# Kernel optimization log

Hardware: AMD Instinct MI355X
Metric: run time of the kernel (lower is better)

## Reference

```python
import jax, jax.numpy as jnp
import numpy as np

PROJ_SCALE = 0.1


def setup_inputs() -> dict:
    key = jax.random.key(0)
    ks = jax.random.split(key, 6)
    B, D, K, E = 8192, 256, 63, 64  # batch, n_features, num_breakpoints, emb_dim_per_feature
    x_num = jax.random.normal(ks[0], (B, D), dtype=jnp.float32)
    basis_weight = jax.random.normal(ks[1], (D, K + 1, E), dtype=jnp.float32) * 0.001
    basis_bias = jnp.zeros((D, E), dtype=jnp.float32)
    proj_w = jax.random.normal(ks[2], (D, D * E), dtype=jnp.float32) * 0.01  # torch Linear weight (out, in)
    proj_b = jnp.zeros((D,), dtype=jnp.float32)
    breakpoint_min = jax.random.normal(ks[3], (D, 1), dtype=jnp.float32) * 0.1
    breakpoint_delta_raw = jax.random.normal(ks[4], (D, K), dtype=jnp.float32) * 0.5
    return {
        "x_num": x_num,
        "basis_weight": basis_weight,
        "basis_bias": basis_bias,
        "proj_w": proj_w,
        "proj_b": proj_b,
        "breakpoint_min": breakpoint_min,
        "breakpoint_delta_raw": breakpoint_delta_raw,
    }


def reference(x_num, basis_weight, basis_bias, proj_w, proj_b, breakpoint_min, breakpoint_delta_raw):
    # breakpoints: monotone via softplus deltas + cumsum, shape [D, K]
    deltas = jax.nn.softplus(breakpoint_delta_raw)
    breakpoints = breakpoint_min + jnp.cumsum(deltas, axis=1)
    # piecewise-linear basis: [B, D, K+1]
    basis = jax.nn.relu(x_num[:, :, None] - breakpoints[None, :, :])
    basis = jnp.concatenate([x_num[:, :, None], basis], axis=-1)
    # per-feature batched matmul: [B, D, E]
    embeddings = jnp.einsum("bdf,dfe->bde", basis, basis_weight) + basis_bias
    flat = embeddings.reshape(x_num.shape[0], -1)  # [B, D*E]
    x_emb = x_num + PROJ_SCALE * (flat @ proj_w.T + proj_b)
    return x_emb, embeddings, breakpoints
```

## Files before the change

kernel.cpp:

```cpp
#include <hip/hip_runtime.h>
#include <hip/hip_bf16.h>

#define NB 8192
#define ND 256
#define NKBP 63
#define NF 64
#define NE 64
#define NKP 16384
#define NDE 16384
#define NSPLIT 8

typedef __attribute__((ext_vector_type(8))) short short8_t;
typedef __attribute__((ext_vector_type(4))) short short4_t;
typedef __attribute__((ext_vector_type(4))) float f32x4;

__device__ __forceinline__ unsigned short bfbits(float v) {
  union { __hip_bfloat16 b; unsigned short u; } cv;
  cv.b = __float2bfloat16(v);
  return cv.u;
}
__device__ __forceinline__ float bf2f(unsigned short s) {
  return __uint_as_float(((unsigned)s) << 16);
}

__global__ void k_maxx(const float* __restrict__ x, float* __restrict__ bmax) {
  const int t = threadIdx.x;
  const float* px = x + (size_t)blockIdx.x * 8192;
  float m = 0.f;
  #pragma unroll 4
  for (int i = t; i < 8192; i += 256) m = fmaxf(m, px[i]);
  #pragma unroll
  for (int off = 32; off > 0; off >>= 1) m = fmaxf(m, __shfl_down(m, off, 64));
  __shared__ float red[4];
  if ((t & 63) == 0) red[t >> 6] = m;
  __syncthreads();
  if (t == 0) bmax[blockIdx.x] = fmaxf(fmaxf(red[0], red[1]), fmaxf(red[2], red[3]));
}

__global__ void k_bp(const float* __restrict__ bmin, const float* __restrict__ draw,
                     const float* __restrict__ bmax, float* __restrict__ obp,
                     int* __restrict__ fdv, int* __restrict__ fcutc) {
  const int d = threadIdx.x;
  __shared__ float mred[256];
  __shared__ int fds[256];
  mred[d] = bmax[d];
  __syncthreads();
  for (int s = 128; s > 0; s >>= 1) {
    if (d < s) mred[d] = fmaxf(mred[d], mred[d + s]);
    __syncthreads();
  }
  const float maxx = mred[0];
  float a = bmin[d];
  int cnt = 0;
  for (int j = 0; j < NKBP; ++j) {
    float r = draw[d * NKBP + j];
    a += fmaxf(r, 0.f) + log1pf(expf(-fabsf(r)));
    obp[d * NKBP + j] = a;
    cnt += (a < maxx) ? 1 : 0;
  }
  const int Fd = 1 + cnt;
  fdv[d] = Fd;
  fds[d] = Fd;
  __syncthreads();
  if (d < NSPLIT) {
    int mx = 0;
    for (int k = 0; k < 32; ++k) mx = max(mx, fds[d * 32 + k]);
    fcutc[d] = (mx > 32) ? 2 : 1;
  }
}

__global__ __launch_bounds__(256, 2) void k_w2(
    const float* __restrict__ bw, const float* __restrict__ pw,
    const float* __restrict__ bb, unsigned short* __restrict__ w2f,
    float* __restrict__ cb_part) {
  const int d = blockIdx.x;
  const int t = threadIdx.x;
  const int l = t & 63, w = t >> 6;
  const int lr = l & 15, lg = l >> 4;
  __shared__ unsigned short pwS[256 * 72];
  __shared__ unsigned short bwS[64 * 72];
  __shared__ float bbS[64];

  {
    const int rr = t >> 4, e0 = (t & 15) * 4;
    #pragma unroll
    for (int it = 0; it < 16; ++it) {
      const int n = it * 16 + rr;
      f32x4 v = *(const f32x4*)(pw + (size_t)n * NDE + d * 64 + e0);
      short4_t s;
      s[0] = (short)bfbits(v[0]); s[1] = (short)bfbits(v[1]);
      s[2] = (short)bfbits(v[2]); s[3] = (short)bfbits(v[3]);
      *(short4_t*)(pwS + n * 72 + e0) = s;
    }
    #pragma unroll
    for (int it = 0; it < 4; ++it) {
      const int f = it * 16 + rr;
      f32x4 v = *(const f32x4*)(bw + (size_t)d * 4096 + f * 64 + e0);
      short4_t s;
      s[0] = (short)bfbits(v[0]); s[1] = (short)bfbits(v[1]);
      s[2] = (short)bfbits(v[2]); s[3] = (short)bfbits(v[3]);
      *(short4_t*)(bwS + f * 72 + e0) = s;
    }
    if (t < 64) bbS[t] = bb[(size_t)d * 64 + t];
  }
  __syncthreads();

  f32x4 acc[4][4];
  #pragma unroll
  for (int mi = 0; mi < 4; ++mi)
    #pragma unroll
    for (int ni = 0; ni < 4; ++ni) acc[mi][ni] = (f32x4){0.f, 0.f, 0.f, 0.f};

  short8_t afr[4][2], bfr[4][2];
  #pragma unroll
  for (int kf = 0; kf < 2; ++kf) {
    #pragma unroll
    for (int mi = 0; mi < 4; ++mi) {
      const int n = w * 64 + mi * 16 + lr;
      afr[mi][kf] = *(const short8_t*)(pwS + n * 72 + kf * 32 + lg * 8);
    }
    #pragma unroll
    for (int ni = 0; ni < 4; ++ni) {
      const int f = ni * 16 + lr;
      bfr[ni][kf] = *(const short8_t*)(bwS + f * 72 + kf * 32 + lg * 8);
    }
  }
  #pragma unroll
  for (int kf = 0; kf < 2; ++kf)
    #pragma unroll
    for (int mi = 0; mi < 4; ++mi)
      #pragma unroll
      for (int ni = 0; ni < 4; ++ni)
        acc[mi][ni] = __builtin_amdgcn_mfma_f32_16x16x32_bf16(afr[mi][kf], bfr[ni][kf], acc[mi][ni], 0, 0, 0);

  #pragma unroll
  for (int mi = 0; mi < 4; ++mi)
    #pragma unroll
    for (int ni = 0; ni < 4; ++ni) {
      const int kf_s = ni >> 1;
      const int lgp  = (ni * 2 + (lr >> 3)) & 3;
      const int jj   = lr & 7;
      const int nb   = w * 64 + mi * 16 + lg * 4;
      const size_t base = (((size_t)d * 2 + kf_s) * 4 + lgp) * 256;
      #pragma unroll
      for (int r = 0; r < 4; ++r)
        w2f[(base + (nb + r)) * 8 + jj] = bfbits(acc[mi][ni][r]);
    }

  {
    float cacc = 0.f;
    #pragma unroll 8
    for (int e = 0; e < 64; ++e) cacc += bf2f(pwS[t * 72 + e]) * bbS[e];
    cb_part[(size_t)d * 256 + t] = cacc;
  }
}

__global__ void k_cbr(const float* __restrict__ cb_part, float* __restrict__ c) {
  const int t = threadIdx.x;
  float a0 = 0.f, a1 = 0.f, a2 = 0.f, a3 = 0.f;
  for (int d = 0; d < ND; d += 4) {
    a0 += cb_part[(size_t)(d + 0) * 256 + t];
    a1 += cb_part[(size_t)(d + 1) * 256 + t];
    a2 += cb_part[(size_t)(d + 2) * 256 + t];
    a3 += cb_part[(size_t)(d + 3) * 256 + t];
  }
  c[t] = (a0 + a1) + (a2 + a3);
}

template<bool KF1>
__device__ __forceinline__ void proj_kloop(
    const unsigned short* const (&bbase)[4], const float* const (&xrow)[2],
    const float* thrS_lg, bool lg0, f32x4 (&acc)[2][4]) {
  for (int c = 0; c < 4; ++c) {
    f32x4 xqa[2], xqb[2];
    #pragma unroll
    for (int mi = 0; mi < 2; ++mi) {
      xqa[mi] = *(const f32x4*)(xrow[mi] + c * 8);
      xqb[mi] = *(const f32x4*)(xrow[mi] + c * 8 + 4);
    }
    #pragma unroll
    for (int dd = 0; dd < 8; ++dd) {
      const int dl = c * 8 + dd;
      short8_t bfr0[4], bfr1[4];
      #pragma unroll
      for (int ni = 0; ni < 4; ++ni)
        bfr0[ni] = *(const short8_t*)(bbase[ni] + (size_t)dl * 16384);
      if (KF1) {
        #pragma unroll
        for (int ni = 0; ni < 4; ++ni)
          bfr1[ni] = *(const short8_t*)(bbase[ni] + (size_t)dl * 16384 + 8192);
      }
      const float* tp = thrS_lg + dl * 64;
      f32x4 ta = *(const f32x4*)(tp);
      f32x4 tb = *(const f32x4*)(tp + 4);
      short8_t afr0[2], afr1[2];
      #pragma unroll
      for (int mi = 0; mi < 2; ++mi) {
        const float xv = (dd < 4) ? xqa[mi][dd & 3] : xqb[mi][dd & 3];
        short8_t A0;
        A0[0] = (short)bfbits(lg0 ? xv : fmaxf(xv - ta[0], 0.f));
        A0[1] = (short)bfbits(fmaxf(xv - ta[1], 0.f));
        A0[2] = (short)bfbits(fmaxf(xv - ta[2], 0.f));
        A0[3] = (short)bfbits(fmaxf(xv - ta[3], 0.f));
        A0[4] = (short)bfbits(fmaxf(xv - tb[0], 0.f));
        A0[5] = (short)bfbits(fmaxf(xv - tb[1], 0.f));
        A0[6] = (short)bfbits(fmaxf(xv - tb[2], 0.f));
        A0[7] = (short)bfbits(fmaxf(xv - tb[3], 0.f));
        afr0[mi] = A0;
      }
      if (KF1) {
        f32x4 tc = *(const f32x4*)(tp + 32);
        f32x4 td = *(const f32x4*)(tp + 36);
        #pragma unroll
        for (int mi = 0; mi < 2; ++mi) {
          const float xv = (dd < 4) ? xqa[mi][dd & 3] : xqb[mi][dd & 3];
          short8_t A1;
          A1[0] = (short)bfbits(fmaxf(xv - tc[0], 0.f));
          A1[1] = (short)bfbits(fmaxf(xv - tc[1], 0.f));
          A1[2] = (short)bfbits(fmaxf(xv - tc[2], 0.f));
          A1[3] = (short)bfbits(fmaxf(xv - tc[3], 0.f));
          A1[4] = (short)bfbits(fmaxf(xv - td[0], 0.f));
          A1[5] = (short)bfbits(fmaxf(xv - td[1], 0.f));
          A1[6] = (short)bfbits(fmaxf(xv - td[2], 0.f));
          A1[7] = (short)bfbits(fmaxf(xv - td[3], 0.f));
          afr1[mi] = A1;
        }
      }
      #pragma unroll
      for (int mi = 0; mi < 2; ++mi)
        #pragma unroll
        for (int ni = 0; ni < 4; ++ni)
          acc[mi][ni] = __builtin_amdgcn_mfma_f32_16x16x32_bf16(afr0[mi], bfr0[ni], acc[mi][ni], 0, 0, 0);
      if (KF1) {
        #pragma unroll
        for (int mi = 0; mi < 2; ++mi)
          #pragma unroll
          for (int ni = 0; ni < 4; ++ni)
            acc[mi][ni] = __builtin_amdgcn_mfma_f32_16x16x32_bf16(afr1[mi], bfr1[ni], acc[mi][ni], 0, 0, 0);
      }
    }
  }
}

__global__ __launch_bounds__(256, 3) void k_proj(
    const unsigned short* __restrict__ w2f, const float* __restrict__ bp,
    const float* __restrict__ x, const int* __restrict__ fcutc,
    float* __restrict__ pbuf) {
  const int t = threadIdx.x;
  const int l = t & 63, w = t >> 6;
  const int lr = l & 15, lg = l >> 4;
  const int bM = blockIdx.x * 128;
  const int bN = blockIdx.y * 64;
  const int d0 = blockIdx.z * 32;
  __shared__ float thrS[32 * 64];

  for (int i = t; i < 2048; i += 256) {
    const int dl = i >> 6, f = i & 63;
    thrS[i] = (f >= 1) ? bp[(size_t)(d0 + dl) * NKBP + f - 1] : 0.0f;
  }
  __syncthreads();

  f32x4 acc[2][4];
  #pragma unroll
  for (int mi = 0; mi < 2; ++mi)
    #pragma unroll
    for (int ni = 0; ni < 4; ++ni) acc[mi][ni] = (f32x4){0.f, 0.f, 0.f, 0.f};

  const bool lg0 = (lg == 0);
  const unsigned short* bbase[4];
  #pragma unroll
  for (int ni = 0; ni < 4; ++ni)
    bbase[ni] = w2f + (size_t)d0 * 16384 + (size_t)(bN + ni * 16 + lr) * 8 + (size_t)lg * 2048;
  const float* xrow[2];
  #pragma unroll
  for (int mi = 0; mi < 2; ++mi)
    xrow[mi] = x + (size_t)(bM + w * 32 + mi * 16 + lr) * ND + d0;

  const int nkf = fcutc[blockIdx.z];
  if (nkf == 1) proj_kloop<false>(bbase, xrow, thrS + lg * 8, lg0, acc);
  else          proj_kloop<true >(bbase, xrow, thrS + lg * 8, lg0, acc);

  float* pp = pbuf + (size_t)blockIdx.z * ((size_t)NB * ND);
  #pragma unroll
  for (int mi = 0; mi < 2; ++mi)
    #pragma unroll
    for (int ni = 0; ni < 4; ++ni) {
      const int col = bN + ni * 16 + lr;
      const int rowb = bM + w * 32 + mi * 16 + lg * 4;
      #pragma unroll
      for (int r = 0; r < 4; ++r)
        pp[(size_t)(rowb + r) * ND + col] = acc[mi][ni][r];
    }
}

__global__ void k_comb(const float* __restrict__ x, const float* __restrict__ pbuf,
                       const float* __restrict__ cbuf, const float* __restrict__ pb,
                       float* __restrict__ xe) {
  const size_t i = ((size_t)blockIdx.x * 256 + threadIdx.x) * 4;
  const int n = (int)(i & 255);
  f32x4 s = *(const f32x4*)(pbuf + i);
  #pragma unroll
  for (int p = 1; p < NSPLIT; ++p)
    s += *(const f32x4*)(pbuf + (size_t)p * 2097152 + i);
  f32x4 cv = *(const f32x4*)(cbuf + n);
  f32x4 pv = *(const f32x4*)(pb + n);
  f32x4 xv = *(const f32x4*)(x + i);
  *(f32x4*)(xe + i) = xv + 0.1f * (s + cv + pv);
}

__global__ __launch_bounds__(256, 2) void k_emb(
    const float* __restrict__ x, const float* __restrict__ bw,
    const float* __restrict__ bb, const float* __restrict__ bp,
    const int* __restrict__ fdv, float* __restrict__ oe) {
  const int d = blockIdx.y;
  const int b0 = blockIdx.x * 256;
  const int t = threadIdx.x;
  const int l = t & 63, w = t >> 6;
  const int lr = l & 15, lg = l >> 4;
  __shared__ unsigned short btS[64 * 72];
  __shared__ float thrF[64];
  __shared__ float bbS[64];
  __shared__ float cS[4 * 64 * 68];

  const int nkf = (fdv[d] > 32) ? 2 : 1;

  float xg[4];
  #pragma unroll
  for (int mi = 0; mi < 4; ++mi)
    xg[mi] = x[(size_t)(b0 + w * 64 + mi * 16 + lr) * ND + d];

  if (t < 64) thrF[t] = (t >= 1) ? bp[(size_t)d * NKBP + t - 1] : 0.0f;
  else if (t < 128) bbS[t - 64] = bb[(size_t)d * 64 + (t - 64)];
  {
    const float* bwd = bw + (size_t)d * 4096;
    const int f = t >> 2, e0 = (t & 3) * 16;
    #pragma unroll
    for (int q = 0; q < 4; ++q) {
      f32x4 v = *(const f32x4*)(bwd + f * 64 + e0 + q * 4);
      #pragma unroll
      for (int r = 0; r < 4; ++r) {
        const int e = e0 + q * 4 + r;
        btS[e * 72 + f] = bfbits(v[r]);
      }
    }
  }
  __syncthreads();

  f32x4 ta = *(const f32x4*)(thrF + lg * 8);
  f32x4 tb = *(const f32x4*)(thrF + lg * 8 + 4);
  const bool lg0 = (lg == 0);

  short8_t afr0[4], afr1[4];
  #pragma unroll
  for (int mi = 0; mi < 4; ++mi) {
    const float xv = xg[mi];
    short8_t A0;
    A0[0] = (short)bfbits(lg0 ? xv : fmaxf(xv - ta[0], 0.f));
    A0[1] = (short)bfbits(fmaxf(xv - ta[1], 0.f));
    A0[2] = (short)bfbits(fmaxf(xv - ta[2], 0.f));
    A0[3] = (short)bfbits(fmaxf(xv - ta[3], 0.f));
    A0[4] = (short)bfbits(fmaxf(xv - tb[0], 0.f));
    A0[5] = (short)bfbits(fmaxf(xv - tb[1], 0.f));
    A0[6] = (short)bfbits(fmaxf(xv - tb[2], 0.f));
    A0[7] = (short)bfbits(fmaxf(xv - tb[3], 0.f));
    afr0[mi] = A0;
  }
  short8_t bfr0[4], bfr1[4];
  #pragma unroll
  for (int ni = 0; ni < 4; ++ni) {
    const int e = ni * 16 + lr;
    bfr0[ni] = *(const short8_t*)(btS + e * 72 + lg * 8);
  }
  f32x4 acc[4][4];
  #pragma unroll
  for (int mi = 0; mi < 4; ++mi)
    #pragma unroll
    for (int ni = 0; ni < 4; ++ni) acc[mi][ni] = (f32x4){0.f, 0.f, 0.f, 0.f};
  #pragma unroll
  for (int mi = 0; mi < 4; ++mi)
    #pragma unroll
    for (int ni = 0; ni < 4; ++ni)
      acc[mi][ni] = __builtin_amdgcn_mfma_f32_16x16x32_bf16(afr0[mi], bfr0[ni], acc[mi][ni], 0, 0, 0);

  if (nkf == 2) {
    f32x4 tc = *(const f32x4*)(thrF + 32 + lg * 8);
    f32x4 td = *(const f32x4*)(thrF + 36 + lg * 8);
    #pragma unroll
    for (int mi = 0; mi < 4; ++mi) {
      const float xv = xg[mi];
      short8_t A1;
      A1[0] = (short)bfbits(fmaxf(xv - tc[0], 0.f));
      A1[1] = (short)bfbits(fmaxf(xv - tc[1], 0.f));
      A1[2] = (short)bfbits(fmaxf(xv - tc[2], 0.f));
      A1[3] = (short)bfbits(fmaxf(xv - tc[3], 0.f));
      A1[4] = (short)bfbits(fmaxf(xv - td[0], 0.f));
      A1[5] = (short)bfbits(fmaxf(xv - td[1], 0.f));
      A1[6] = (short)bfbits(fmaxf(xv - td[2], 0.f));
      A1[7] = (short)bfbits(fmaxf(xv - td[3], 0.f));
      afr1[mi] = A1;
    }
    #pragma unroll
    for (int ni = 0; ni < 4; ++ni) {
      const int e = ni * 16 + lr;
      bfr1[ni] = *(const short8_t*)(btS + e * 72 + 32 + lg * 8);
    }
    #pragma unroll
    for (int mi = 0; mi < 4; ++mi)
      #pragma unroll
      for (int ni = 0; ni < 4; ++ni)
        acc[mi][ni] = __builtin_amdgcn_mfma_f32_16x16x32_bf16(afr1[mi], bfr1[ni], acc[mi][ni], 0, 0, 0);
  }

  #pragma unroll
  for (int ni = 0; ni < 4; ++ni) {
    const float bbv = bbS[ni * 16 + lr];
    #pragma unroll
    for (int mi = 0; mi < 4; ++mi) {
      const int rw = mi * 16 + lg * 4;
      #pragma unroll
      for (int r = 0; r < 4; ++r)
        cS[w * 4352 + (rw + r) * 68 + ni * 16 + lr] = acc[mi][ni][r] + bbv;
    }
  }
  __syncthreads();

  const int rsub = t >> 4;
  const int c4 = (t & 15) * 4;
  #pragma unroll
  for (int p = 0; p < 16; ++p) {
    const int row = p * 16 + rsub;
    const int wsrc = row >> 6, wr = row & 63;
    f32x4 v = *(const f32x4*)(cS + wsrc * 4352 + wr * 68 + c4);
    *(f32x4*)(oe + (size_t)(b0 + row) * NDE + d * 64 + c4) = v;
  }
}

extern "C" void kernel_launch(void* const* d_in, const int* in_sizes, int n_in,
                              void* d_out, int out_size, void* d_ws, size_t ws_size,
                              hipStream_t stream) {
  const float* x    = (const float*)d_in[0];
  const float* bw   = (const float*)d_in[1];
  const float* bb   = (const float*)d_in[2];
  const float* pw   = (const float*)d_in[3];
  const float* pb   = (const float*)d_in[4];
  const float* bmin = (const float*)d_in[5];
  const float* draw = (const float*)d_in[6];

  float* out    = (float*)d_out;
  float* out_x  = out;
  float* out_e  = out + (size_t)NB * ND;
  float* out_bp = out_e + (size_t)NB * NDE;

  unsigned short* w2f = (unsigned short*)out_x;
  float* cbuf    = out_e;
  float* pbuf    = out_e + 65536;
  float* cb_part = out_e + 65536 + NSPLIT * 2097152;
  float* bmax = (float*)d_ws;
  int*   fdv  = (int*)d_ws + 256;
  int*   fcutc= (int*)d_ws + 512;

  k_maxx<<<dim3(256),          dim3(256), 0, stream>>>(x, bmax);
  k_bp  <<<dim3(1),            dim3(256), 0, stream>>>(bmin, draw, bmax, out_bp, fdv, fcutc);
  k_w2  <<<dim3(256),          dim3(256), 0, stream>>>(bw, pw, bb, w2f, cb_part);
  k_cbr <<<dim3(1),            dim3(256), 0, stream>>>(cb_part, cbuf);
  k_proj<<<dim3(64, 4, NSPLIT),dim3(256), 0, stream>>>(w2f, out_bp, x, fcutc, pbuf);
  k_comb<<<dim3(2048),         dim3(256), 0, stream>>>(x, pbuf, cbuf, pb, out_x);
  k_emb <<<dim3(32, 256),      dim3(256), 0, stream>>>(x, bw, bb, out_bp, fdv, out_e);
}
```

Before: 264.7 us.

## Skip unused K chunks in k_w2, prefetch proj B fragments, shrink k_emb tiles

k_w2 now reads the per-group K cutoff and loads and multiplies only the basis rows needed, skipping the second K half when breakpoints beyond the data max are irrelevant. proj_kloop double-buffers the global B-fragment loads so the next feature's weights are fetched while the current MFMAs run. k_emb halves its batch tile to 128 rows, raises occupancy to 3 blocks per SM, and drops the block barrier by having each wave store its own rows. The cost is more registers for the prefetch buffers, runtime loops that replace unrolled ones, and twice as many k_emb blocks.

```diff
diff --git a/kernel.cpp b/kernel.cpp
--- a/kernel.cpp
+++ b/kernel.cpp
@@ -71,12 +71,13 @@
 
 __global__ __launch_bounds__(256, 2) void k_w2(
     const float* __restrict__ bw, const float* __restrict__ pw,
-    const float* __restrict__ bb, unsigned short* __restrict__ w2f,
-    float* __restrict__ cb_part) {
+    const float* __restrict__ bb, const int* __restrict__ fcutc,
+    unsigned short* __restrict__ w2f, float* __restrict__ cb_part) {
   const int d = blockIdx.x;
   const int t = threadIdx.x;
   const int l = t & 63, w = t >> 6;
   const int lr = l & 15, lg = l >> 4;
+  const int nkf = fcutc[d >> 5];
   __shared__ unsigned short pwS[256 * 72];
   __shared__ unsigned short bwS[64 * 72];
   __shared__ float bbS[64];
@@ -92,8 +93,8 @@
       s[2] = (short)bfbits(v[2]); s[3] = (short)bfbits(v[3]);
       *(short4_t*)(pwS + n * 72 + e0) = s;
     }
-    #pragma unroll
-    for (int it = 0; it < 4; ++it) {
+    const int itmax = (nkf == 2) ? 4 : 2;
+    for (int it = 0; it < itmax; ++it) {
       const int f = it * 16 + rr;
       f32x4 v = *(const f32x4*)(bw + (size_t)d * 4096 + f * 64 + e0);
       short4_t s;
@@ -111,32 +112,27 @@
     #pragma unroll
     for (int ni = 0; ni < 4; ++ni) acc[mi][ni] = (f32x4){0.f, 0.f, 0.f, 0.f};
 
-  short8_t afr[4][2], bfr[4][2];
-  #pragma unroll
-  for (int kf = 0; kf < 2; ++kf) {
+  const int nimax = (nkf == 2) ? 4 : 2;
+  for (int kf = 0; kf < nkf; ++kf) {
+    short8_t afr[4], bfr[4];
     #pragma unroll
     for (int mi = 0; mi < 4; ++mi) {
       const int n = w * 64 + mi * 16 + lr;
-      afr[mi][kf] = *(const short8_t*)(pwS + n * 72 + kf * 32 + lg * 8);
-    }
-    #pragma unroll
-    for (int ni = 0; ni < 4; ++ni) {
+      afr[mi] = *(const short8_t*)(pwS + n * 72 + kf * 32 + lg * 8);
+    }
+    for (int ni = 0; ni < nimax; ++ni) {
       const int f = ni * 16 + lr;
-      bfr[ni][kf] = *(const short8_t*)(bwS + f * 72 + kf * 32 + lg * 8);
-    }
-  }
-  #pragma unroll
-  for (int kf = 0; kf < 2; ++kf)
-    #pragma unroll
-    for (int mi = 0; mi < 4; ++mi)
-      #pragma unroll
-      for (int ni = 0; ni < 4; ++ni)
-        acc[mi][ni] = __builtin_amdgcn_mfma_f32_16x16x32_bf16(afr[mi][kf], bfr[ni][kf], acc[mi][ni], 0, 0, 0);
+      bfr[ni] = *(const short8_t*)(bwS + f * 72 + kf * 32 + lg * 8);
+    }
+    for (int ni = 0; ni < nimax; ++ni)
+      #pragma unroll
+      for (int mi = 0; mi < 4; ++mi)
+        acc[mi][ni] = __builtin_amdgcn_mfma_f32_16x16x32_bf16(afr[mi], bfr[ni], acc[mi][ni], 0, 0, 0);
+  }
 
   #pragma unroll
   for (int mi = 0; mi < 4; ++mi)
-    #pragma unroll
-    for (int ni = 0; ni < 4; ++ni) {
+    for (int ni = 0; ni < nimax; ++ni) {
       const int kf_s = ni >> 1;
       const int lgp  = (ni * 2 + (lr >> 3)) & 3;
       const int jj   = lr & 7;
@@ -171,6 +167,12 @@
 __device__ __forceinline__ void proj_kloop(
     const unsigned short* const (&bbase)[4], const float* const (&xrow)[2],
     const float* thrS_lg, bool lg0, f32x4 (&acc)[2][4]) {
+  short8_t bcur[2][4], bnxt[2][4];
+  #pragma unroll
+  for (int ni = 0; ni < 4; ++ni) {
+    bcur[0][ni] = *(const short8_t*)(bbase[ni]);
+    if (KF1) bcur[1][ni] = *(const short8_t*)(bbase[ni] + 8192);
+  }
   for (int c = 0; c < 4; ++c) {
     f32x4 xqa[2], xqb[2];
     #pragma unroll
@@ -181,14 +183,11 @@
     #pragma unroll
     for (int dd = 0; dd < 8; ++dd) {
       const int dl = c * 8 + dd;
-      short8_t bfr0[4], bfr1[4];
-      #pragma unroll
-      for (int ni = 0; ni < 4; ++ni)
-        bfr0[ni] = *(const short8_t*)(bbase[ni] + (size_t)dl * 16384);
-      if (KF1) {
-        #pragma unroll
-        for (int ni = 0; ni < 4; ++ni)
-          bfr1[ni] = *(const short8_t*)(bbase[ni] + (size_t)dl * 16384 + 8192);
+      const int nxt = (dl + 1 < 32) ? dl + 1 : dl;
+      #pragma unroll
+      for (int ni = 0; ni < 4; ++ni) {
+        bnxt[0][ni] = *(const short8_t*)(bbase[ni] + (size_t)nxt * 16384);
+        if (KF1) bnxt[1][ni] = *(const short8_t*)(bbase[ni] + (size_t)nxt * 16384 + 8192);
       }
       const float* tp = thrS_lg + dl * 64;
       f32x4 ta = *(const f32x4*)(tp);
@@ -230,13 +229,18 @@
       for (int mi = 0; mi < 2; ++mi)
         #pragma unroll
         for (int ni = 0; ni < 4; ++ni)
-          acc[mi][ni] = __builtin_amdgcn_mfma_f32_16x16x32_bf16(afr0[mi], bfr0[ni], acc[mi][ni], 0, 0, 0);
+          acc[mi][ni] = __builtin_amdgcn_mfma_f32_16x16x32_bf16(afr0[mi], bcur[0][ni], acc[mi][ni], 0, 0, 0);
       if (KF1) {
         #pragma unroll
         for (int mi = 0; mi < 2; ++mi)
           #pragma unroll
           for (int ni = 0; ni < 4; ++ni)
-            acc[mi][ni] = __builtin_amdgcn_mfma_f32_16x16x32_bf16(afr1[mi], bfr1[ni], acc[mi][ni], 0, 0, 0);
+            acc[mi][ni] = __builtin_amdgcn_mfma_f32_16x16x32_bf16(afr1[mi], bcur[1][ni], acc[mi][ni], 0, 0, 0);
+      }
+      #pragma unroll
+      for (int ni = 0; ni < 4; ++ni) {
+        bcur[0][ni] = bnxt[0][ni];
+        if (KF1) bcur[1][ni] = bnxt[1][ni];
       }
     }
   }
@@ -308,26 +312,26 @@
   *(f32x4*)(xe + i) = xv + 0.1f * (s + cv + pv);
 }
 
-__global__ __launch_bounds__(256, 2) void k_emb(
+__global__ __launch_bounds__(256, 3) void k_emb(
     const float* __restrict__ x, const float* __restrict__ bw,
     const float* __restrict__ bb, const float* __restrict__ bp,
     const int* __restrict__ fdv, float* __restrict__ oe) {
   const int d = blockIdx.y;
-  const int b0 = blockIdx.x * 256;
+  const int b0 = blockIdx.x * 128;
   const int t = threadIdx.x;
   const int l = t & 63, w = t >> 6;
   const int lr = l & 15, lg = l >> 4;
   __shared__ unsigned short btS[64 * 72];
   __shared__ float thrF[64];
   __shared__ float bbS[64];
-  __shared__ float cS[4 * 64 * 68];
+  __shared__ float cS[4 * 32 * 68];
 
   const int nkf = (fdv[d] > 32) ? 2 : 1;
 
-  float xg[4];
-  #pragma unroll
-  for (int mi = 0; mi < 4; ++mi)
-    xg[mi] = x[(size_t)(b0 + w * 64 + mi * 16 + lr) * ND + d];
+  float xg[2];
+  #pragma unroll
+  for (int mi = 0; mi < 2; ++mi)
+    xg[mi] = x[(size_t)(b0 + w * 32 + mi * 16 + lr) * ND + d];
 
   if (t < 64) thrF[t] = (t >= 1) ? bp[(size_t)d * NKBP + t - 1] : 0.0f;
   else if (t < 128) bbS[t - 64] = bb[(size_t)d * 64 + (t - 64)];
@@ -350,9 +354,9 @@
   f32x4 tb = *(const f32x4*)(thrF + lg * 8 + 4);
   const bool lg0 = (lg == 0);
 
-  short8_t afr0[4], afr1[4];
-  #pragma unroll
-  for (int mi = 0; mi < 4; ++mi) {
+  short8_t afr0[2];
+  #pragma unroll
+  for (int mi = 0; mi < 2; ++mi) {
     const float xv = xg[mi];
     short8_t A0;
     A0[0] = (short)bfbits(lg0 ? xv : fmaxf(xv - ta[0], 0.f));
@@ -365,19 +369,19 @@
     A0[7] = (short)bfbits(fmaxf(xv - tb[3], 0.f));
     afr0[mi] = A0;
   }
-  short8_t bfr0[4], bfr1[4];
+  short8_t bfr0[4];
   #pragma unroll
   for (int ni = 0; ni < 4; ++ni) {
     const int e = ni * 16 + lr;
     bfr0[ni] = *(const short8_t*)(btS + e * 72 + lg * 8);
   }
-  f32x4 acc[4][4];
-  #pragma unroll
-  for (int mi = 0; mi < 4; ++mi)
+  f32x4 acc[2][4];
+  #pragma unroll
+  for (int mi = 0; mi < 2; ++mi)
     #pragma unroll
     for (int ni = 0; ni < 4; ++ni) acc[mi][ni] = (f32x4){0.f, 0.f, 0.f, 0.f};
   #pragma unroll
-  for (int mi = 0; mi < 4; ++mi)
+  for (int mi = 0; mi < 2; ++mi)
     #pragma unroll
     for (int ni = 0; ni < 4; ++ni)
       acc[mi][ni] = __builtin_amdgcn_mfma_f32_16x16x32_bf16(afr0[mi], bfr0[ni], acc[mi][ni], 0, 0, 0);
@@ -385,8 +389,10 @@
   if (nkf == 2) {
     f32x4 tc = *(const f32x4*)(thrF + 32 + lg * 8);
     f32x4 td = *(const f32x4*)(thrF + 36 + lg * 8);
-    #pragma unroll
-    for (int mi = 0; mi < 4; ++mi) {
+    short8_t afr1[2];
+    short8_t bfr1[4];
+    #pragma unroll
+    for (int mi = 0; mi < 2; ++mi) {
       const float xv = xg[mi];
       short8_t A1;
       A1[0] = (short)bfbits(fmaxf(xv - tc[0], 0.f));
@@ -405,7 +411,7 @@
       bfr1[ni] = *(const short8_t*)(btS + e * 72 + 32 + lg * 8);
     }
     #pragma unroll
-    for (int mi = 0; mi < 4; ++mi)
+    for (int mi = 0; mi < 2; ++mi)
       #pragma unroll
       for (int ni = 0; ni < 4; ++ni)
         acc[mi][ni] = __builtin_amdgcn_mfma_f32_16x16x32_bf16(afr1[mi], bfr1[ni], acc[mi][ni], 0, 0, 0);
@@ -415,23 +421,21 @@
   for (int ni = 0; ni < 4; ++ni) {
     const float bbv = bbS[ni * 16 + lr];
     #pragma unroll
-    for (int mi = 0; mi < 4; ++mi) {
+    for (int mi = 0; mi < 2; ++mi) {
       const int rw = mi * 16 + lg * 4;
       #pragma unroll
       for (int r = 0; r < 4; ++r)
-        cS[w * 4352 + (rw + r) * 68 + ni * 16 + lr] = acc[mi][ni][r] + bbv;
-    }
-  }
-  __syncthreads();
-
-  const int rsub = t >> 4;
-  const int c4 = (t & 15) * 4;
-  #pragma unroll
-  for (int p = 0; p < 16; ++p) {
-    const int row = p * 16 + rsub;
-    const int wsrc = row >> 6, wr = row & 63;
-    f32x4 v = *(const f32x4*)(cS + wsrc * 4352 + wr * 68 + c4);
-    *(f32x4*)(oe + (size_t)(b0 + row) * NDE + d * 64 + c4) = v;
+        cS[w * 2176 + (rw + r) * 68 + ni * 16 + lr] = acc[mi][ni][r] + bbv;
+    }
+  }
+
+  const int rsub = l >> 4;
+  const int c4 = (l & 15) * 4;
+  #pragma unroll
+  for (int p = 0; p < 8; ++p) {
+    const int rl = p * 4 + rsub;
+    f32x4 v = *(const f32x4*)(cS + w * 2176 + rl * 68 + c4);
+    *(f32x4*)(oe + (size_t)(b0 + w * 32 + rl) * NDE + d * 64 + c4) = v;
   }
 }
 
@@ -461,9 +465,9 @@
 
   k_maxx<<<dim3(256),          dim3(256), 0, stream>>>(x, bmax);
   k_bp  <<<dim3(1),            dim3(256), 0, stream>>>(bmin, draw, bmax, out_bp, fdv, fcutc);
-  k_w2  <<<dim3(256),          dim3(256), 0, stream>>>(bw, pw, bb, w2f, cb_part);
+  k_w2  <<<dim3(256),          dim3(256), 0, stream>>>(bw, pw, bb, fcutc, w2f, cb_part);
   k_cbr <<<dim3(1),            dim3(256), 0, stream>>>(cb_part, cbuf);
   k_proj<<<dim3(64, 4, NSPLIT),dim3(256), 0, stream>>>(w2f, out_bp, x, fcutc, pbuf);
   k_comb<<<dim3(2048),         dim3(256), 0, stream>>>(x, pbuf, cbuf, pb, out_x);
-  k_emb <<<dim3(32, 256),      dim3(256), 0, stream>>>(x, bw, bb, out_bp, fdv, out_e);
-}
+  k_emb <<<dim3(64, 256),      dim3(256), 0, stream>>>(x, bw, bb, out_bp, fdv, out_e);
+}
```

Result: slower. 316.8 us (+19.6%).

## Pre-pack bf16 basis weights and thresholds for direct fragment loads in k_emb

Applied to the files above, without the earlier changes.

Adds a k_prep kernel that converts basis weights to bf16 once, in the MFMA fragment layout, and has k_bp write a padded threshold table. k_emb can then load B fragments and thresholds straight from global memory, dropping the per-block transpose through shared memory and shrinking its epilogue staging buffer so three blocks fit per CU. k_w2 also skips the second K-slice when the breakpoint cut shows it is unused. The fast path depends on the workspace being large enough, and keeps a fallback kernel otherwise.

```diff
diff --git a/kernel.cpp b/kernel.cpp
--- a/kernel.cpp
+++ b/kernel.cpp
@@ -39,7 +39,8 @@
 
 __global__ void k_bp(const float* __restrict__ bmin, const float* __restrict__ draw,
                      const float* __restrict__ bmax, float* __restrict__ obp,
-                     int* __restrict__ fdv, int* __restrict__ fcutc) {
+                     int* __restrict__ fdv, int* __restrict__ fcutc,
+                     float* __restrict__ thrT) {
   const int d = threadIdx.x;
   __shared__ float mred[256];
   __shared__ int fds[256];
@@ -52,10 +53,12 @@
   const float maxx = mred[0];
   float a = bmin[d];
   int cnt = 0;
+  if (thrT) thrT[d * 64] = 0.0f;
   for (int j = 0; j < NKBP; ++j) {
     float r = draw[d * NKBP + j];
     a += fmaxf(r, 0.f) + log1pf(expf(-fabsf(r)));
     obp[d * NKBP + j] = a;
+    if (thrT) thrT[d * 64 + 1 + j] = a;
     cnt += (a < maxx) ? 1 : 0;
   }
   const int Fd = 1 + cnt;
@@ -69,14 +72,30 @@
   }
 }
 
+__global__ void k_prep(const float* __restrict__ bw, unsigned short* __restrict__ bwT) {
+  const int d = blockIdx.x;
+  const int t = threadIdx.x;
+  const int f = t >> 2, e0 = (t & 3) * 16;
+  const int kf = f >> 5, lg = (f >> 3) & 3, j = f & 7;
+  const size_t base = ((((size_t)d * 2 + kf) * 4 + lg) * 64) * 8 + j;
+  #pragma unroll
+  for (int q = 0; q < 4; ++q) {
+    f32x4 v = *(const f32x4*)(bw + (size_t)d * 4096 + f * 64 + e0 + q * 4);
+    #pragma unroll
+    for (int r = 0; r < 4; ++r)
+      bwT[base + (size_t)(e0 + q * 4 + r) * 8] = bfbits(v[r]);
+  }
+}
+
 __global__ __launch_bounds__(256, 2) void k_w2(
     const float* __restrict__ bw, const float* __restrict__ pw,
-    const float* __restrict__ bb, unsigned short* __restrict__ w2f,
-    float* __restrict__ cb_part) {
+    const float* __restrict__ bb, const int* __restrict__ fcutc,
+    unsigned short* __restrict__ w2f, float* __restrict__ cb_part) {
   const int d = blockIdx.x;
   const int t = threadIdx.x;
   const int l = t & 63, w = t >> 6;
   const int lr = l & 15, lg = l >> 4;
+  const int nkf = fcutc[d >> 5];
   __shared__ unsigned short pwS[256 * 72];
   __shared__ unsigned short bwS[64 * 72];
   __shared__ float bbS[64];
@@ -92,8 +111,8 @@
       s[2] = (short)bfbits(v[2]); s[3] = (short)bfbits(v[3]);
       *(short4_t*)(pwS + n * 72 + e0) = s;
     }
-    #pragma unroll
-    for (int it = 0; it < 4; ++it) {
+    const int itmax = (nkf == 2) ? 4 : 2;
+    for (int it = 0; it < itmax; ++it) {
       const int f = it * 16 + rr;
       f32x4 v = *(const f32x4*)(bw + (size_t)d * 4096 + f * 64 + e0);
       short4_t s;
@@ -111,32 +130,27 @@
     #pragma unroll
     for (int ni = 0; ni < 4; ++ni) acc[mi][ni] = (f32x4){0.f, 0.f, 0.f, 0.f};
 
-  short8_t afr[4][2], bfr[4][2];
-  #pragma unroll
-  for (int kf = 0; kf < 2; ++kf) {
+  const int nimax = (nkf == 2) ? 4 : 2;
+  for (int kf = 0; kf < nkf; ++kf) {
+    short8_t afr[4], bfr[4];
     #pragma unroll
     for (int mi = 0; mi < 4; ++mi) {
       const int n = w * 64 + mi * 16 + lr;
-      afr[mi][kf] = *(const short8_t*)(pwS + n * 72 + kf * 32 + lg * 8);
-    }
-    #pragma unroll
-    for (int ni = 0; ni < 4; ++ni) {
+      afr[mi] = *(const short8_t*)(pwS + n * 72 + kf * 32 + lg * 8);
+    }
+    for (int ni = 0; ni < nimax; ++ni) {
       const int f = ni * 16 + lr;
-      bfr[ni][kf] = *(const short8_t*)(bwS + f * 72 + kf * 32 + lg * 8);
-    }
-  }
-  #pragma unroll
-  for (int kf = 0; kf < 2; ++kf)
-    #pragma unroll
-    for (int mi = 0; mi < 4; ++mi)
-      #pragma unroll
-      for (int ni = 0; ni < 4; ++ni)
-        acc[mi][ni] = __builtin_amdgcn_mfma_f32_16x16x32_bf16(afr[mi][kf], bfr[ni][kf], acc[mi][ni], 0, 0, 0);
-
-  #pragma unroll
-  for (int mi = 0; mi < 4; ++mi)
-    #pragma unroll
-    for (int ni = 0; ni < 4; ++ni) {
+      bfr[ni] = *(const short8_t*)(bwS + f * 72 + kf * 32 + lg * 8);
+    }
+    for (int ni = 0; ni < nimax; ++ni)
+      #pragma unroll
+      for (int mi = 0; mi < 4; ++mi)
+        acc[mi][ni] = __builtin_amdgcn_mfma_f32_16x16x32_bf16(afr[mi], bfr[ni], acc[mi][ni], 0, 0, 0);
+  }
+
+  #pragma unroll
+  for (int mi = 0; mi < 4; ++mi)
+    for (int ni = 0; ni < nimax; ++ni) {
       const int kf_s = ni >> 1;
       const int lgp  = (ni * 2 + (lr >> 3)) & 3;
       const int jj   = lr & 7;
@@ -308,7 +322,118 @@
   *(f32x4*)(xe + i) = xv + 0.1f * (s + cv + pv);
 }
 
-__global__ __launch_bounds__(256, 2) void k_emb(
+__global__ __launch_bounds__(256, 3) void k_emb(
+    const float* __restrict__ x, const unsigned short* __restrict__ bwT,
+    const float* __restrict__ bb, const float* __restrict__ thrT,
+    const int* __restrict__ fdv, float* __restrict__ oe) {
+  const int d = blockIdx.y;
+  const int b0 = blockIdx.x * 256;
+  const int t = threadIdx.x;
+  const int l = t & 63, w = t >> 6;
+  const int lr = l & 15, lg = l >> 4;
+  __shared__ float cS[4 * 32 * 68];
+
+  const int nkf = (fdv[d] > 32) ? 2 : 1;
+
+  float xg[4];
+  #pragma unroll
+  for (int mi = 0; mi < 4; ++mi)
+    xg[mi] = x[(size_t)(b0 + w * 64 + mi * 16 + lr) * ND + d];
+
+  f32x4 ta = *(const f32x4*)(thrT + d * 64 + lg * 8);
+  f32x4 tb = *(const f32x4*)(thrT + d * 64 + lg * 8 + 4);
+  const bool lg0 = (lg == 0);
+
+  float bbv[4];
+  #pragma unroll
+  for (int ni = 0; ni < 4; ++ni) bbv[ni] = bb[(size_t)d * 64 + ni * 16 + lr];
+
+  const unsigned short* bk0 = bwT + ((size_t)d * 8 + lg) * 512;
+  short8_t bfr0[4];
+  #pragma unroll
+  for (int ni = 0; ni < 4; ++ni)
+    bfr0[ni] = *(const short8_t*)(bk0 + (ni * 16 + lr) * 8);
+
+  short8_t afr0[4];
+  #pragma unroll
+  for (int mi = 0; mi < 4; ++mi) {
+    const float xv = xg[mi];
+    short8_t A0;
+    A0[0] = (short)bfbits(lg0 ? xv : fmaxf(xv - ta[0], 0.f));
+    A0[1] = (short)bfbits(fmaxf(xv - ta[1], 0.f));
+    A0[2] = (short)bfbits(fmaxf(xv - ta[2], 0.f));
+    A0[3] = (short)bfbits(fmaxf(xv - ta[3], 0.f));
+    A0[4] = (short)bfbits(fmaxf(xv - tb[0], 0.f));
+    A0[5] = (short)bfbits(fmaxf(xv - tb[1], 0.f));
+    A0[6] = (short)bfbits(fmaxf(xv - tb[2], 0.f));
+    A0[7] = (short)bfbits(fmaxf(xv - tb[3], 0.f));
+    afr0[mi] = A0;
+  }
+
+  f32x4 acc[4][4];
+  #pragma unroll
+  for (int mi = 0; mi < 4; ++mi)
+    #pragma unroll
+    for (int ni = 0; ni < 4; ++ni) acc[mi][ni] = (f32x4){0.f, 0.f, 0.f, 0.f};
+  #pragma unroll
+  for (int mi = 0; mi < 4; ++mi)
+    #pragma unroll
+    for (int ni = 0; ni < 4; ++ni)
+      acc[mi][ni] = __builtin_amdgcn_mfma_f32_16x16x32_bf16(afr0[mi], bfr0[ni], acc[mi][ni], 0, 0, 0);
+
+  if (nkf == 2) {
+    f32x4 tc = *(const f32x4*)(thrT + d * 64 + 32 + lg * 8);
+    f32x4 td = *(const f32x4*)(thrT + d * 64 + 36 + lg * 8);
+    const unsigned short* bk1 = bwT + ((size_t)d * 8 + 4 + lg) * 512;
+    short8_t afr1[4], bfr1[4];
+    #pragma unroll
+    for (int ni = 0; ni < 4; ++ni)
+      bfr1[ni] = *(const short8_t*)(bk1 + (ni * 16 + lr) * 8);
+    #pragma unroll
+    for (int mi = 0; mi < 4; ++mi) {
+      const float xv = xg[mi];
+      short8_t A1;
+      A1[0] = (short)bfbits(fmaxf(xv - tc[0], 0.f));
+      A1[1] = (short)bfbits(fmaxf(xv - tc[1], 0.f));
+      A1[2] = (short)bfbits(fmaxf(xv - tc[2], 0.f));
+      A1[3] = (short)bfbits(fmaxf(xv - tc[3], 0.f));
+      A1[4] = (short)bfbits(fmaxf(xv - td[0], 0.f));
+      A1[5] = (short)bfbits(fmaxf(xv - td[1], 0.f));
+      A1[6] = (short)bfbits(fmaxf(xv - td[2], 0.f));
+      A1[7] = (short)bfbits(fmaxf(xv - td[3], 0.f));
+      afr1[mi] = A1;
+    }
+    #pragma unroll
+    for (int mi = 0; mi < 4; ++mi)
+      #pragma unroll
+      for (int ni = 0; ni < 4; ++ni)
+        acc[mi][ni] = __builtin_amdgcn_mfma_f32_16x16x32_bf16(afr1[mi], bfr1[ni], acc[mi][ni], 0, 0, 0);
+  }
+
+  const int rsub = l >> 4;
+  const int c4 = (l & 15) * 4;
+  #pragma unroll
+  for (int half = 0; half < 2; ++half) {
+    #pragma unroll
+    for (int ni = 0; ni < 4; ++ni) {
+      #pragma unroll
+      for (int mi = 0; mi < 2; ++mi) {
+        const int rw = mi * 16 + lg * 4;
+        #pragma unroll
+        for (int r = 0; r < 4; ++r)
+          cS[w * 2176 + (rw + r) * 68 + ni * 16 + lr] = acc[half * 2 + mi][ni][r] + bbv[ni];
+      }
+    }
+    #pragma unroll
+    for (int p = 0; p < 8; ++p) {
+      const int rl = p * 4 + rsub;
+      f32x4 v = *(const f32x4*)(cS + w * 2176 + rl * 68 + c4);
+      *(f32x4*)(oe + (size_t)(b0 + w * 64 + half * 32 + rl) * NDE + d * 64 + c4) = v;
+    }
+  }
+}
+
+__global__ __launch_bounds__(256, 2) void k_emb_fb(
     const float* __restrict__ x, const float* __restrict__ bw,
     const float* __restrict__ bb, const float* __restrict__ bp,
     const int* __restrict__ fdv, float* __restrict__ oe) {
@@ -323,7 +448,6 @@
   __shared__ float cS[4 * 64 * 68];
 
   const int nkf = (fdv[d] > 32) ? 2 : 1;
-
   float xg[4];
   #pragma unroll
   for (int mi = 0; mi < 4; ++mi)
@@ -350,7 +474,7 @@
   f32x4 tb = *(const f32x4*)(thrF + lg * 8 + 4);
   const bool lg0 = (lg == 0);
 
-  short8_t afr0[4], afr1[4];
+  short8_t afr0[4];
   #pragma unroll
   for (int mi = 0; mi < 4; ++mi) {
     const float xv = xg[mi];
@@ -365,7 +489,7 @@
     A0[7] = (short)bfbits(fmaxf(xv - tb[3], 0.f));
     afr0[mi] = A0;
   }
-  short8_t bfr0[4], bfr1[4];
+  short8_t bfr0[4];
   #pragma unroll
   for (int ni = 0; ni < 4; ++ni) {
     const int e = ni * 16 + lr;
@@ -385,6 +509,7 @@
   if (nkf == 2) {
     f32x4 tc = *(const f32x4*)(thrF + 32 + lg * 8);
     f32x4 td = *(const f32x4*)(thrF + 36 + lg * 8);
+    short8_t afr1[4], bfr1[4];
     #pragma unroll
     for (int mi = 0; mi < 4; ++mi) {
       const float xv = xg[mi];
@@ -455,15 +580,26 @@
   float* cbuf    = out_e;
   float* pbuf    = out_e + 65536;
   float* cb_part = out_e + 65536 + NSPLIT * 2097152;
-  float* bmax = (float*)d_ws;
-  int*   fdv  = (int*)d_ws + 256;
-  int*   fcutc= (int*)d_ws + 512;
+
+  float* wsf  = (float*)d_ws;
+  float* bmax = wsf;
+  int*   fdv  = (int*)wsf + 256;
+  int*   fcutc= (int*)wsf + 512;
+  float* thrT = wsf + 768;
+  unsigned short* bwT = (unsigned short*)(wsf + 768 + 16384);
+  const bool FAST = ws_size >= (size_t)(768 + 16384) * 4 + (size_t)2097152 * 2 + 256;
 
   k_maxx<<<dim3(256),          dim3(256), 0, stream>>>(x, bmax);
-  k_bp  <<<dim3(1),            dim3(256), 0, stream>>>(bmin, draw, bmax, out_bp, fdv, fcutc);
-  k_w2  <<<dim3(256),          dim3(256), 0, stream>>>(bw, pw, bb, w2f, cb_part);
+  k_bp  <<<dim3(1),            dim3(256), 0, stream>>>(bmin, draw, bmax, out_bp, fdv, fcutc,
+                                                       FAST ? thrT : (float*)nullptr);
+  if (FAST)
+    k_prep<<<dim3(256),        dim3(256), 0, stream>>>(bw, bwT);
+  k_w2  <<<dim3(256),          dim3(256), 0, stream>>>(bw, pw, bb, fcutc, w2f, cb_part);
   k_cbr <<<dim3(1),            dim3(256), 0, stream>>>(cb_part, cbuf);
   k_proj<<<dim3(64, 4, NSPLIT),dim3(256), 0, stream>>>(w2f, out_bp, x, fcutc, pbuf);
   k_comb<<<dim3(2048),         dim3(256), 0, stream>>>(x, pbuf, cbuf, pb, out_x);
-  k_emb <<<dim3(32, 256),      dim3(256), 0, stream>>>(x, bw, bb, out_bp, fdv, out_e);
-}
+  if (FAST)
+    k_emb <<<dim3(32, 256),    dim3(256), 0, stream>>>(x, bwT, bb, thrT, fdv, out_e);
+  else
+    k_emb_fb<<<dim3(32, 256),  dim3(256), 0, stream>>>(x, bw, bb, out_bp, fdv, out_e);
+}
```

New measurement: 265.7 us. No clear change (+0.4%).
